# Optimization experiments

Hardware: AMD Instinct MI355X
Metric: run time of the kernel (lower is better)

## Reference

```python
import jax, jax.numpy as jnp
import numpy as np

N_NODES = 100000
N_EDGES = 1600000
N_HIDDEN = 128
N_CLASSES = 64
K = 10
LN_EPS = 1e-5


def _layer_norm_1d(x):
    # nn.LayerNorm(num_nodes, elementwise_affine=False) over a (N,) vector
    m = jnp.mean(x)
    v = jnp.mean((x - m) ** 2)
    return (x - m) / jnp.sqrt(v + LN_EPS)


def setup_inputs() -> dict:
    key = jax.random.key(0)
    k1, k2, k3, k4, k5 = jax.random.split(key, 5)
    feat = jax.random.normal(k1, (N_NODES, N_HIDDEN), dtype=jnp.float32)
    logits = jax.random.normal(k2, (N_NODES, N_CLASSES), dtype=jnp.float32)
    w_y = jax.random.normal(k3, (N_HIDDEN, N_CLASSES), dtype=jnp.float32) * 0.05
    b_y = jnp.zeros((N_CLASSES,), dtype=jnp.float32)
    tau_1 = jnp.full((1,), 0.5, dtype=jnp.float32)  # reset_parameters, lidx=1
    tau_2 = jnp.full((1,), 0.5, dtype=jnp.float32)
    src = jax.random.randint(k4, (N_EDGES,), 0, N_NODES, dtype=jnp.int32)
    dst = jax.random.randint(k5, (N_EDGES,), 0, N_NODES, dtype=jnp.int32)
    return {"feat": feat, "logits": logits, "w_y": w_y, "b_y": b_y,
            "tau_1": tau_1, "tau_2": tau_2, "src": src, "dst": dst, "k": K}


def reference(feat, logits, w_y, b_y, tau_1, tau_2, src, dst, k):
    N, _ = feat.shape
    C = logits.shape[1]
    # in-degree (also used as nodes.data['degree']), clamped at 1 like the original
    deg = jax.ops.segment_sum(jnp.ones_like(dst, dtype=jnp.float32), dst, num_segments=N)
    deg_c = jnp.maximum(deg, 1.0)
    norm = (deg_c ** -0.5)[:, None]  # (N,1)

    z = jnp.ones((1,), dtype=feat.dtype)
    for lidx in range(k):
        feat = feat * norm
        old_feat = feat
        if lidx != 0:
            logits = feat @ w_y + b_y
        pred = jnp.argmax(logits, axis=1)  # (N,) per-node argmax prediction
        # f1: fraction of in-neighbors agreeing with the center prediction
        eq = (pred[src] == pred[dst]).astype(jnp.float32)  # (E,)
        f1 = jax.ops.segment_sum(eq, dst, num_segments=N) / deg_c
        # f2: entropy of the per-neighborhood class histogram
        onehot = jax.nn.one_hot(pred[src], C, dtype=jnp.float32)  # (E,C)
        cnts = jax.ops.segment_sum(onehot, dst, num_segments=N) / deg_c[:, None]
        cnts = jnp.maximum(cnts, 1e-5)
        f2 = -jnp.sum(cnts * jnp.log(cnts), axis=1)
        f1 = jax.lax.stop_gradient(f1)
        f2 = jax.lax.stop_gradient(f2)
        z = jax.nn.sigmoid(-(_layer_norm_1d(f1) - tau_1)) * \
            jax.nn.sigmoid(-(_layer_norm_1d(f2) - tau_2))  # (N,)
        # SpMM aggregation: h[dst] += feat[src] (edge weights are all ones)
        agg = jax.ops.segment_sum(feat[src], dst, num_segments=N)
        feat = agg * norm
        feat = z[:, None] * feat + old_feat
    return feat
```

## Files before the change

kernel.cpp:

```cpp
#include <hip/hip_runtime.h>
#include <hip/hip_fp16.h>
#include <cstdint>
#include <cstddef>

#define H 128
#define C 64
#define KITER 10
#define SCHUNK 4096


__global__ void k_zero(int* __restrict__ deg, double* __restrict__ stats, int n, int nstats) {
    int i = blockIdx.x * blockDim.x + threadIdx.x;
    if (i < n) deg[i] = 0;
    if (i < nstats) stats[i] = 0.0;
}

__global__ void k_degcount(const int* __restrict__ dst, int* __restrict__ deg, int E) {
    int e = blockIdx.x * blockDim.x + threadIdx.x;
    if (e < E) atomicAdd(&deg[dst[e]], 1);
}


__global__ __launch_bounds__(256) void k_blocksum(const int* __restrict__ deg,
                                                  int* __restrict__ bsum, int n) {
    __shared__ int red[256];
    int t = threadIdx.x;
    int i = blockIdx.x * 256 + t;
    red[t] = (i < n) ? deg[i] : 0;
    __syncthreads();
    for (int off = 128; off >= 1; off >>= 1) {
        if (t < off) red[t] += red[t + off];
        __syncthreads();
    }
    if (t == 0) bsum[blockIdx.x] = red[0];
}

__global__ __launch_bounds__(512) void k_scanb(const int* __restrict__ bsum,
                                               int* __restrict__ boff,
                                               int* __restrict__ row_ptr, int nb, int n) {
    __shared__ int s[512];
    int t = threadIdx.x;
    int v = (t < nb) ? bsum[t] : 0;
    s[t] = v;
    __syncthreads();
    for (int off = 1; off < 512; off <<= 1) {
        int u = (t >= off) ? s[t - off] : 0;
        __syncthreads();
        s[t] += u;
        __syncthreads();
    }
    if (t < nb) boff[t] = s[t] - v;
    if (t == 511) row_ptr[n] = s[511];
}

__global__ __launch_bounds__(256) void k_fill(const int* __restrict__ deg,
                                              const int* __restrict__ boff,
                                              int* __restrict__ row_ptr,
                                              int* __restrict__ row_cur, int n) {
    __shared__ int s[256];
    int t = threadIdx.x;
    int i = blockIdx.x * 256 + t;
    int d = (i < n) ? deg[i] : 0;
    s[t] = d;
    __syncthreads();
    for (int off = 1; off < 256; off <<= 1) {
        int u = (t >= off) ? s[t - off] : 0;
        __syncthreads();
        s[t] += u;
        __syncthreads();
    }
    if (i < n) {
        int base = boff[blockIdx.x] + s[t] - d;
        row_ptr[i] = base;
        row_cur[i] = base;
    }
}

__global__ void k_norm(const int* __restrict__ deg, float* __restrict__ degc,
                       float* __restrict__ nrm, int n) {
    int i = blockIdx.x * blockDim.x + threadIdx.x;
    if (i < n) {
        int d = deg[i];
        float dc = (float)(d > 1 ? d : 1);
        degc[i] = dc;
        nrm[i] = (float)(1.0 / sqrt((double)dc));
    }
}

__global__ __launch_bounds__(256) void k_scatter8(const int* __restrict__ src,
                                                  const int* __restrict__ dst,
                                                  int* __restrict__ row_cur,
                                                  int* __restrict__ csr_src,
                                                  int E, int slice_sz) {
    int chunk = blockIdx.x >> 3;
    int xcd = blockIdx.x & 7;
    int base = chunk * SCHUNK;
    int lo_node = xcd * slice_sz;
    int hi_node = lo_node + slice_sz;
    #pragma unroll
    for (int r = 0; r < SCHUNK; r += 256) {
        int e = base + r + threadIdx.x;
        if (e < E) {
            int d = dst[e];
            if (d >= lo_node && d < hi_node) {
                int pos = atomicAdd(&row_cur[d], 1);
                csr_src[pos] = src[e];
            }
        }
    }
}

__device__ inline uint32_t pack_h2(float x, float y) {
    __half2 h = __floats2half2_rn(x, y);
    return __builtin_bit_cast(uint32_t, h);
}
__device__ inline float2 unpack_h2(uint32_t p) {
    __half2 h = __builtin_bit_cast(__half2, p);
    return __half22float2(h);
}

__global__ __launch_bounds__(256) void k_scale(const float* __restrict__ feat,
                                               const float* __restrict__ nrm,
                                               float* __restrict__ featn,
                                               uint32_t* __restrict__ mir, int n4) {
    int i = blockIdx.x * blockDim.x + threadIdx.x;
    if (i >= n4) return;
    int node = i >> 5;
    float nn = nrm[node];
    float4 v = ((const float4*)feat)[i];
    v.x *= nn; v.y *= nn; v.z *= nn; v.w *= nn;
    ((float4*)featn)[i] = v;
    mir[i * 2]     = pack_h2(v.x, v.y);
    mir[i * 2 + 1] = pack_h2(v.z, v.w);
}


__global__ __launch_bounds__(256) void k_pred0(const float* __restrict__ logits,
                                               int* __restrict__ pred, int n) {
    int wid = (blockIdx.x * blockDim.x + threadIdx.x) >> 6;
    int lane = threadIdx.x & 63;
    if (wid >= n) return;
    float v = logits[(size_t)wid * C + lane];
    int idx = lane;
    #pragma unroll
    for (int off = 1; off < 64; off <<= 1) {
        float ov = __shfl_xor(v, off);
        int oi = __shfl_xor(idx, off);
        if (ov > v || (ov == v && oi < idx)) { v = ov; idx = oi; }
    }
    if (lane == 0) pred[wid] = idx;
}

__global__ __launch_bounds__(256) void k_predG(const float* __restrict__ featn,
                                               const float* __restrict__ w_y,
                                               const float* __restrict__ b_y,
                                               int* __restrict__ pred, int n) {
    int node = blockIdx.x * blockDim.x + threadIdx.x;
    bool act = node < n;
    int ld = act ? node : 0;
    const float4* p4 = (const float4*)(featn + (size_t)ld * H);
    float fv[H];
    #pragma unroll
    for (int q = 0; q < H / 4; ++q) {
        float4 t = p4[q];
        fv[q * 4 + 0] = t.x;
        fv[q * 4 + 1] = t.y;
        fv[q * 4 + 2] = t.z;
        fv[q * 4 + 3] = t.w;
    }
    float best = -3.402823466e+38f;
    int bi = 0;
    for (int cb = 0; cb < C / 8; ++cb) {
        float acc[8];
        #pragma unroll
        for (int u = 0; u < 8; ++u) acc[u] = 0.f;
        const float* wp = w_y + cb * 8;
        #pragma unroll
        for (int h = 0; h < H; ++h) {
            #pragma unroll
            for (int u = 0; u < 8; ++u)
                acc[u] = fmaf(fv[h], wp[h * C + u], acc[u]);
        }
        #pragma unroll
        for (int u = 0; u < 8; ++u) {
            float val = acc[u] + b_y[cb * 8 + u];
            int c = cb * 8 + u;
            if (val > best) { best = val; bi = c; }
        }
    }
    if (act) pred[node] = bi;
}

__global__ __launch_bounds__(256) void k_edge(const int* __restrict__ row_ptr,
                                              const int* __restrict__ csr_src,
                                              const int* __restrict__ pred,
                                              const float* __restrict__ degc,
                                              float* __restrict__ f1, float* __restrict__ f2,
                                              double* __restrict__ stats_iter, int n) {
    __shared__ unsigned char hist[256][64];
    __shared__ double red[256];
    int t = threadIdx.x;
    int node = blockIdx.x * 256 + t;
    uint32_t* hp = (uint32_t*)hist[t];
    #pragma unroll
    for (int q = 0; q < 16; ++q) hp[q] = 0u;
    float v1 = 0.f, v2 = 0.f;
    bool act = node < n;
    if (act) {
        int lo = row_ptr[node], hi = row_ptr[node + 1];
        int pc = pred[node];
        int eq = 0;
        for (int j = lo; j < hi; ++j) {
            int p = pred[csr_src[j]];
            eq += (p == pc) ? 1 : 0;
            hist[t][p] += 1;
        }
        float dc = degc[node];
        v1 = (float)eq / dc;
        float s = 0.f;
        #pragma unroll
        for (int c = 0; c < 64; ++c) {
            float cv = (float)hist[t][c] / dc;
            cv = fmaxf(cv, 1e-5f);
            s += cv * logf(cv);
        }
        v2 = -s;
        f1[node] = v1;
        f2[node] = v2;
    }
    double vals[4];
    vals[0] = act ? (double)v1 : 0.0;
    vals[1] = act ? (double)v1 * (double)v1 : 0.0;
    vals[2] = act ? (double)v2 : 0.0;
    vals[3] = act ? (double)v2 * (double)v2 : 0.0;
    for (int q = 0; q < 4; ++q) {
        red[t] = vals[q];
        __syncthreads();
        for (int off = 128; off >= 1; off >>= 1) {
            if (t < off) red[t] += red[t + off];
            __syncthreads();
        }
        if (t == 0) atomicAdd(&stats_iter[q], red[0]);
        __syncthreads();
    }
}

__global__ __launch_bounds__(256) void k_spmm(const float* __restrict__ featn,
                                              const uint32_t* __restrict__ mir_cur,
                                              float* __restrict__ nxt,
                                              uint32_t* __restrict__ mir_nxt,
                                              const float* __restrict__ nrm,
                                              const int* __restrict__ row_ptr,
                                              const int* __restrict__ csr_src,
                                              const float* __restrict__ f1,
                                              const float* __restrict__ f2,
                                              const double* __restrict__ stats_iter,
                                              const float* __restrict__ tau1,
                                              const float* __restrict__ tau2,
                                              int n, double dN, int last) {
    int wid = (blockIdx.x * blockDim.x + threadIdx.x) >> 6;
    int lane = threadIdx.x & 63;
    if (wid >= n) return;
    int node = __builtin_amdgcn_readfirstlane(wid);

    double S1 = stats_iter[0], Q1 = stats_iter[1];
    double S2 = stats_iter[2], Q2 = stats_iter[3];
    double m1 = S1 / dN, m2 = S2 / dN;
    double rs1 = 1.0 / sqrt(Q1 / dN - m1 * m1 + 1e-5);
    double rs2 = 1.0 / sqrt(Q2 / dN - m2 * m2 + 1e-5);
    float ln1 = (float)(((double)f1[node] - m1) * rs1);
    float ln2 = (float)(((double)f2[node] - m2) * rs2);
    float z1 = 1.f / (1.f + expf(ln1 - tau1[0]));
    float z2 = 1.f / (1.f + expf(ln2 - tau2[0]));
    float z = z1 * z2;

    float nr = nrm[node];
    int lo = row_ptr[node], hi = row_ptr[node + 1];
    float ax = 0.f, ay = 0.f;
    const uint32_t* basep = mir_cur + lane;
    int j = lo;
    for (; j + 3 < hi; j += 4) {
        int s0 = csr_src[j];
        int s1 = csr_src[j + 1];
        int s2 = csr_src[j + 2];
        int s3 = csr_src[j + 3];
        uint32_t p0 = basep[(size_t)s0 * 64];
        uint32_t p1 = basep[(size_t)s1 * 64];
        uint32_t p2 = basep[(size_t)s2 * 64];
        uint32_t p3 = basep[(size_t)s3 * 64];
        float2 f0 = unpack_h2(p0); ax += f0.x; ay += f0.y;
        float2 g1 = unpack_h2(p1); ax += g1.x; ay += g1.y;
        float2 g2 = unpack_h2(p2); ax += g2.x; ay += g2.y;
        float2 g3 = unpack_h2(p3); ax += g3.x; ay += g3.y;
    }
    for (; j < hi; ++j) {
        int s0 = csr_src[j];
        float2 f0 = unpack_h2(basep[(size_t)s0 * 64]);
        ax += f0.x; ay += f0.y;
    }
    const float2 ownn = *(const float2*)(featn + (size_t)node * H + lane * 2);
    float ox = fmaf(z, ax * nr, ownn.x);
    float oy = fmaf(z, ay * nr, ownn.y);
    if (!last) {
        ox *= nr; oy *= nr;
        mir_nxt[(size_t)node * 64 + lane] = pack_h2(ox, oy);
    }
    float2 o; o.x = ox; o.y = oy;
    *(float2*)(nxt + (size_t)node * H + lane * 2) = o;
}


extern "C" void kernel_launch(void* const* d_in, const int* in_sizes, int n_in,
                              void* d_out, int out_size, void* d_ws, size_t ws_size,
                              hipStream_t stream) {
    const float* feat   = (const float*)d_in[0];
    const float* logits = (const float*)d_in[1];
    const float* w_y    = (const float*)d_in[2];
    const float* b_y    = (const float*)d_in[3];
    const float* tau1   = (const float*)d_in[4];
    const float* tau2   = (const float*)d_in[5];
    const int*   src    = (const int*)d_in[6];
    const int*   dst    = (const int*)d_in[7];

    const int N = in_sizes[0] / H;
    const int E = in_sizes[6];
    float* out = (float*)d_out;

    char* ws = (char*)d_ws;
    size_t off = 0;
    auto carve = [&](size_t bytes) -> char* {
        char* p = ws + off;
        off = (off + bytes + 255) & ~(size_t)255;
        return p;
    };
    float*    featnA  = (float*)carve((size_t)N * H * sizeof(float));
    float*    featnB  = (float*)carve((size_t)N * H * sizeof(float));
    uint32_t* mirA    = (uint32_t*)carve((size_t)N * (H / 2) * sizeof(uint32_t));
    uint32_t* mirB    = (uint32_t*)carve((size_t)N * (H / 2) * sizeof(uint32_t));
    float*    nrm     = (float*)carve((size_t)N * sizeof(float));
    float*    degc    = (float*)carve((size_t)N * sizeof(float));
    int*      pred    = (int*)  carve((size_t)N * sizeof(int));
    float*    f1      = (float*)carve((size_t)N * sizeof(float));
    float*    f2      = (float*)carve((size_t)N * sizeof(float));
    int*      deg     = (int*)  carve((size_t)N * sizeof(int));
    int*      row_ptr = (int*)  carve((size_t)(N + 1) * sizeof(int));
    int*      row_cur = (int*)  carve((size_t)N * sizeof(int));
    int*      bsum    = (int*)  carve((size_t)1024 * sizeof(int));
    int*      csr_src = (int*)  carve((size_t)E * sizeof(int));
    double*   stats   = (double*)carve((size_t)KITER * 8 * sizeof(double));

    const int TB = 256;
    int gN = (N + TB - 1) / TB;
    int gE = (E + TB - 1) / TB;

    k_zero<<<gN, TB, 0, stream>>>(deg, stats, N, KITER * 8);
    k_degcount<<<gE, TB, 0, stream>>>(dst, deg, E);
    k_blocksum<<<gN, TB, 0, stream>>>(deg, bsum, N);
    k_scanb<<<1, 512, 0, stream>>>(bsum, bsum + 512, row_ptr, gN, N);
    k_fill<<<gN, TB, 0, stream>>>(deg, bsum + 512, row_ptr, row_cur, N);
    k_norm<<<gN, TB, 0, stream>>>(deg, degc, nrm, N);
    int nchunk = (E + SCHUNK - 1) / SCHUNK;
    int slice_sz = (N + 7) / 8;
    k_scatter8<<<nchunk * 8, TB, 0, stream>>>(src, dst, row_cur, csr_src, E, slice_sz);
    int n4 = N * (H / 4);
    k_scale<<<(n4 + TB - 1) / TB, TB, 0, stream>>>(feat, nrm, featnA, mirA, n4);

    const float* cur = featnA;
    const uint32_t* mcur = mirA;
    int gWave = (N + 3) / 4;
    for (int l = 0; l < KITER; ++l) {
        int last = (l == KITER - 1);
        float* nxt = last ? out : ((l % 2 == 0) ? featnB : featnA);
        uint32_t* mnxt = (l % 2 == 0) ? mirB : mirA;
        if (l == 0)
            k_pred0<<<gWave, TB, 0, stream>>>(logits, pred, N);
        else
            k_predG<<<gN, TB, 0, stream>>>(cur, w_y, b_y, pred, N);
        k_edge<<<gN, TB, 0, stream>>>(row_ptr, csr_src, pred, degc, f1, f2,
                                      stats + (size_t)l * 8, N);
        k_spmm<<<gWave, TB, 0, stream>>>(cur, mcur, nxt, mnxt, nrm, row_ptr, csr_src,
                                         f1, f2, stats + (size_t)l * 8, tau1, tau2,
                                         N, (double)N, last);
        cur = nxt;
        mcur = mnxt;
    }
}
```

Measured before the change: 1.822 ms.

## Compute neighborhood histogram with one wavefront per node and split stats reduction

The edge-feature kernel now assigns one 64-lane wavefront per node, with each lane counting how many neighbors predict its class. The entropy comes from a shuffle reduction, and the agreement count is read from the center class's lane. This removes the per-thread shared-memory byte histograms and the serial per-thread 64-class entropy loop. The mean/variance statistics move to a separate grid-stride reduction kernel, which adds a launch and a reread of f1/f2. Every lane loads each neighbor's prediction redundantly, though these are broadcast loads.

```diff
diff --git a/kernel.cpp b/kernel.cpp
--- a/kernel.cpp
+++ b/kernel.cpp
@@ -191,48 +191,53 @@
     if (act) pred[node] = bi;
 }
 
-__global__ __launch_bounds__(256) void k_edge(const int* __restrict__ row_ptr,
-                                              const int* __restrict__ csr_src,
-                                              const int* __restrict__ pred,
-                                              const float* __restrict__ degc,
-                                              float* __restrict__ f1, float* __restrict__ f2,
-                                              double* __restrict__ stats_iter, int n) {
-    __shared__ unsigned char hist[256][64];
+__global__ __launch_bounds__(256) void k_edgew(const int* __restrict__ row_ptr,
+                                               const int* __restrict__ csr_src,
+                                               const int* __restrict__ pred,
+                                               const float* __restrict__ degc,
+                                               float* __restrict__ f1,
+                                               float* __restrict__ f2, int n) {
+    int wid = (blockIdx.x * blockDim.x + threadIdx.x) >> 6;
+    int lane = threadIdx.x & 63;
+    if (wid >= n) return;
+    int node = __builtin_amdgcn_readfirstlane(wid);
+    int lo = __builtin_amdgcn_readfirstlane(row_ptr[node]);
+    int hi = __builtin_amdgcn_readfirstlane(row_ptr[node + 1]);
+    int pc = pred[node];
+    int cnt = 0;
+    for (int j = lo; j < hi; ++j) {
+        int s = csr_src[j];
+        int p = pred[s];
+        cnt += (p == lane) ? 1 : 0;
+    }
+    float dc = degc[node];
+    float cv = (float)cnt / dc;
+    cv = fmaxf(cv, 1e-5f);
+    float term = cv * logf(cv);
+    #pragma unroll
+    for (int off = 1; off < 64; off <<= 1) term += __shfl_xor(term, off);
+    float v2 = -term;
+    int eq = __shfl(cnt, pc);
+    float v1 = (float)eq / dc;
+    if (lane == 0) {
+        f1[node] = v1;
+        f2[node] = v2;
+    }
+}
+
+__global__ __launch_bounds__(256) void k_stats(const float* __restrict__ f1,
+                                               const float* __restrict__ f2,
+                                               double* __restrict__ stats_iter, int n) {
     __shared__ double red[256];
     int t = threadIdx.x;
-    int node = blockIdx.x * 256 + t;
-    uint32_t* hp = (uint32_t*)hist[t];
-    #pragma unroll
-    for (int q = 0; q < 16; ++q) hp[q] = 0u;
-    float v1 = 0.f, v2 = 0.f;
-    bool act = node < n;
-    if (act) {
-        int lo = row_ptr[node], hi = row_ptr[node + 1];
-        int pc = pred[node];
-        int eq = 0;
-        for (int j = lo; j < hi; ++j) {
-            int p = pred[csr_src[j]];
-            eq += (p == pc) ? 1 : 0;
-            hist[t][p] += 1;
-        }
-        float dc = degc[node];
-        v1 = (float)eq / dc;
-        float s = 0.f;
-        #pragma unroll
-        for (int c = 0; c < 64; ++c) {
-            float cv = (float)hist[t][c] / dc;
-            cv = fmaxf(cv, 1e-5f);
-            s += cv * logf(cv);
-        }
-        v2 = -s;
-        f1[node] = v1;
-        f2[node] = v2;
-    }
-    double vals[4];
-    vals[0] = act ? (double)v1 : 0.0;
-    vals[1] = act ? (double)v1 * (double)v1 : 0.0;
-    vals[2] = act ? (double)v2 : 0.0;
-    vals[3] = act ? (double)v2 * (double)v2 : 0.0;
+    double s1 = 0.0, q1 = 0.0, s2 = 0.0, q2 = 0.0;
+    for (int i = blockIdx.x * 256 + t; i < n; i += gridDim.x * 256) {
+        double a = (double)f1[i];
+        double b = (double)f2[i];
+        s1 += a; q1 += a * a;
+        s2 += b; q2 += b * b;
+    }
+    double vals[4] = {s1, q1, s2, q2};
     for (int q = 0; q < 4; ++q) {
         red[t] = vals[q];
         __syncthreads();
@@ -376,8 +381,8 @@
             k_pred0<<<gWave, TB, 0, stream>>>(logits, pred, N);
         else
             k_predG<<<gN, TB, 0, stream>>>(cur, w_y, b_y, pred, N);
-        k_edge<<<gN, TB, 0, stream>>>(row_ptr, csr_src, pred, degc, f1, f2,
-                                      stats + (size_t)l * 8, N);
+        k_edgew<<<gWave, TB, 0, stream>>>(row_ptr, csr_src, pred, degc, f1, f2, N);
+        k_stats<<<256, TB, 0, stream>>>(f1, f2, stats + (size_t)l * 8, N);
         k_spmm<<<gWave, TB, 0, stream>>>(cur, mcur, nxt, mnxt, nrm, row_ptr, csr_src,
                                          f1, f2, stats + (size_t)l * 8, tau1, tau2,
                                          N, (double)N, last);
```

After: 2.208 ms. 21.2% more time.
